# Performance work log

Measured on AMD Instinct MI355X. Metric: run time of the kernel, lower is better.

## Reference

```python
import jax, jax.numpy as jnp
import numpy as np

NUM_HEADS = 16
D_MODEL = 1024
HEAD_DIM = D_MODEL // NUM_HEADS
SCALE = float(np.sqrt(HEAD_DIM))  # NOTE: original multiplies q by sqrt(head_dim)
EPS = 1e-5


def layernorm(x, g, b):
    # LayerNorm over last dim (head_dim), learnable affine
    mu = jnp.mean(x, axis=-1, keepdims=True)
    var = jnp.mean(jnp.square(x - mu), axis=-1, keepdims=True)
    return (x - mu) * jax.lax.rsqrt(var + EPS) * g + b


def setup_inputs() -> dict:
    key = jax.random.key(0)
    ks = jax.random.split(key, 8)
    B, Nq, Nc = 2, 2048, 2048
    s = 0.02
    return {
        "x_query": jax.random.normal(ks[0], (B, Nq, D_MODEL), jnp.float32),
        "x_context": jax.random.normal(ks[1], (B, Nc, D_MODEL), jnp.float32),
        "Wq": jax.random.normal(ks[2], (D_MODEL, D_MODEL), jnp.float32) * s,
        "Wkv": jax.random.normal(ks[3], (D_MODEL, 2 * D_MODEL), jnp.float32) * s,
        "Wp": jax.random.normal(ks[4], (D_MODEL, D_MODEL), jnp.float32) * s,
        "bp": jnp.zeros((D_MODEL,), jnp.float32),
        "ln_g": jnp.ones((HEAD_DIM,), jnp.float32),
        "ln_b": jnp.zeros((HEAD_DIM,), jnp.float32),
    }


def reference(x_query, x_context, Wq, Wkv, Wp, bp, ln_g, ln_b):
    B, Nq, _ = x_query.shape
    Nc = x_context.shape[1]
    H, D = NUM_HEADS, HEAD_DIM
    # projections
    q = (x_query @ Wq).reshape(B, Nq, H, D).transpose(0, 2, 1, 3)  # b h n d
    kv = (x_context @ Wkv).reshape(B, Nc, 2, H, D)
    k = kv[:, :, 0].transpose(0, 2, 1, 3)  # b h n d
    v = kv[:, :, 1].transpose(0, 2, 1, 3)
    # QK-LayerNorm (shared params)
    q = layernorm(q, ln_g, ln_b)
    k = layernorm(k, ln_g, ln_b)
    # NOTE: faithful to source — q is MULTIPLIED by sqrt(head_dim)
    q = q * SCALE
    attn = jnp.einsum("bhqd,bhkd->bhqk", q, k)
    attn = jax.nn.softmax(attn, axis=-1)
    out = jnp.einsum("bhqk,bhkd->bhqd", attn, v)
    out = out.transpose(0, 2, 1, 3).reshape(B, Nq, H * D)
    return out @ Wp + bp
```

## Files before the change

### kernel.cpp

```cpp
#include <hip/hip_runtime.h>
#include <stdint.h>

#define NUM_HEADS 16
#define HEAD_DIM 64
#define D_MODEL 1024
#define SEQ 2048
#define BATCH 2

typedef unsigned short u16;
typedef _Float16 f16x8 __attribute__((ext_vector_type(8)));
typedef float f32x4 __attribute__((ext_vector_type(4)));

__device__ __forceinline__ u16 f2h(float f) {
    _Float16 h = (_Float16)f;
    return __builtin_bit_cast(u16, h);
}
__device__ __forceinline__ float h2f(u16 h) {
    return (float)__builtin_bit_cast(_Float16, h);
}
__device__ __forceinline__ uint32_t pkrtz(float a, float b) {
    return __builtin_bit_cast(uint32_t, __builtin_amdgcn_cvt_pkrtz(a, b));
}
__device__ __forceinline__ uint32_t pkrtn(float a, float b) {
    return (uint32_t)f2h(a) | ((uint32_t)f2h(b) << 16);
}

__device__ __forceinline__ float ex2(float x) {
#if __has_builtin(__builtin_amdgcn_exp2f)
    return __builtin_amdgcn_exp2f(x);
#else
    float r;
    asm("v_exp_f32 %0, %1" : "=v"(r) : "v"(x));
    return r;
#endif
}

__device__ __forceinline__ f16x8 ld8h(const u16* p) {
    return *reinterpret_cast<const f16x8*>(p);
}

__device__ __forceinline__ void gl_lds16(const void* g, void* l) {
    __builtin_amdgcn_global_load_lds(
        (const __attribute__((address_space(1))) void*)g,
        (__attribute__((address_space(3))) void*)l,
        16, 0, 0);
}

template <int CTRL>
__device__ __forceinline__ float dpp_mov(float x) {
    return __builtin_bit_cast(float,
        __builtin_amdgcn_update_dpp(0, __builtin_bit_cast(int, x), CTRL, 0xf, 0xf, true));
}
__device__ __forceinline__ float rowsum16(float x) {
    x += dpp_mov<0x121>(x);
    x += dpp_mov<0x122>(x);
    x += dpp_mov<0x124>(x);
    x += dpp_mov<0x128>(x);
    return x;
}

__global__ __launch_bounds__(256) void k_prep(const float* __restrict__ xq,
                                              const float* __restrict__ xc,
                                              const float* __restrict__ Wq,
                                              const float* __restrict__ Wkv,
                                              const float* __restrict__ Wp,
                                              u16* __restrict__ xq16,
                                              u16* __restrict__ xc16,
                                              u16* __restrict__ WqT16,
                                              u16* __restrict__ WkvT16,
                                              u16* __restrict__ WpT16) {
    __shared__ float tile[32][33];
    const int t = blockIdx.x;
    if (t < 8192) {
        int i = t * 256 + threadIdx.x;
        const float* src; u16* dst; int j;
        if (i < 1048576) { src = xq; dst = xq16; j = i; }
        else             { src = xc; dst = xc16; j = i - 1048576; }
        float4 v = reinterpret_cast<const float4*>(src)[j];
        ushort4 o;
        o.x = f2h(v.x); o.y = f2h(v.y); o.z = f2h(v.z); o.w = f2h(v.w);
        reinterpret_cast<ushort4*>(dst)[j] = o;
        return;
    }
    const float* W; u16* WT; int N, bi;
    if (t < 9216)       { W = Wq;  WT = WqT16;  N = 1024; bi = t - 8192; }
    else if (t < 11264) { W = Wkv; WT = WkvT16; N = 2048; bi = t - 9216; }
    else                { W = Wp;  WT = WpT16;  N = 1024; bi = t - 11264; }
    const int K = 1024;
    const int nb = N / 32;
    const int bn = (bi % nb) * 32, bk = (bi / nb) * 32;
    const int tx = threadIdx.x & 31;
    const int ty = threadIdx.x >> 5;
#pragma unroll
    for (int i = 0; i < 32; i += 8)
        tile[ty + i][tx] = W[(size_t)(bk + ty + i) * N + bn + tx];
    __syncthreads();
#pragma unroll
    for (int i = 0; i < 32; i += 8)
        WT[(size_t)(bn + ty + i) * K + bk + tx] = f2h(tile[tx][ty + i]);
}

__device__ __forceinline__ void gemm_mainloop_f16(const u16* __restrict__ A,
                                                  const u16* __restrict__ Bt,
                                                  u16* As, u16* Bs,
                                                  int tileM, int tileN, int K,
                                                  f32x4 acc[4][4]) {
    const int tid = threadIdx.x;
    const int lane = tid & 63;
    const int wv = tid >> 6;
    const int wm = wv >> 1, wn = wv & 1;
    const int quad = lane >> 4, l15 = lane & 15;

    const int c0 = tid, c1 = tid + 256;
    const u16* Ap0 = A + (size_t)(tileM + (c0 >> 2)) * K + (c0 & 3) * 8;
    const u16* Ap1 = A + (size_t)(tileM + (c1 >> 2)) * K + (c1 & 3) * 8;
    const u16* Bp0 = Bt + (size_t)(tileN + (c0 >> 2)) * K + (c0 & 3) * 8;
    const u16* Bp1 = Bt + (size_t)(tileN + (c1 >> 2)) * K + (c1 & 3) * 8;

    gl_lds16(Ap0, &As[c0 * 8]);
    gl_lds16(Ap1, &As[c1 * 8]);
    gl_lds16(Bp0, &Bs[c0 * 8]);
    gl_lds16(Bp1, &Bs[c1 * 8]);

    for (int k0 = 0; k0 < K; k0 += 32) {
        __syncthreads();
        const int cb = (k0 >> 5) & 1;
        if (k0 + 32 < K) {
            const int nbuf = cb ^ 1;
            gl_lds16(Ap0 + k0 + 32, &As[nbuf * 4096 + c0 * 8]);
            gl_lds16(Ap1 + k0 + 32, &As[nbuf * 4096 + c1 * 8]);
            gl_lds16(Bp0 + k0 + 32, &Bs[nbuf * 4096 + c0 * 8]);
            gl_lds16(Bp1 + k0 + 32, &Bs[nbuf * 4096 + c1 * 8]);
        }
        const int cbo = cb * 4096;
        f16x8 af[4], bfr[4];
#pragma unroll
        for (int mi = 0; mi < 4; ++mi)
            af[mi] = ld8h(&As[cbo + (wm * 64 + mi * 16 + l15) * 32 + quad * 8]);
#pragma unroll
        for (int ni = 0; ni < 4; ++ni)
            bfr[ni] = ld8h(&Bs[cbo + (wn * 64 + ni * 16 + l15) * 32 + quad * 8]);
#pragma unroll
        for (int mi = 0; mi < 4; ++mi)
#pragma unroll
            for (int ni = 0; ni < 4; ++ni)
                acc[mi][ni] = __builtin_amdgcn_mfma_f32_16x16x32_f16(
                    af[mi], bfr[ni], acc[mi][ni], 0, 0, 0);
    }
}

#define ACC_INIT()                                                   \
    f32x4 acc[4][4];                                                 \
    _Pragma("unroll") for (int i = 0; i < 4; ++i)                    \
        _Pragma("unroll") for (int j = 0; j < 4; ++j)                \
            acc[i][j] = (f32x4){0.f, 0.f, 0.f, 0.f};

__global__ __launch_bounds__(256, 2) void k_proj_f16(const u16* __restrict__ xq16,
                                                     const u16* __restrict__ xc16,
                                                     const u16* __restrict__ WqT16,
                                                     const u16* __restrict__ WkvT16,
                                                     const float* __restrict__ lng,
                                                     const float* __restrict__ lnb,
                                                     u16* __restrict__ Qh_h,
                                                     u16* __restrict__ Qh_l,
                                                     u16* __restrict__ Kh,
                                                     u16* __restrict__ VT) {
    __shared__ __align__(16) u16 As[2 * 128 * 32];
    __shared__ __align__(16) u16 Bs[2 * 128 * 32];
    const int bx = blockIdx.x;
    const int tileM = blockIdx.y * 128;
    const int tid = threadIdx.x;
    const int lane = tid & 63;
    const int wv = tid >> 6;
    const int wm = wv >> 1, wn = wv & 1;
    const int quad = lane >> 4, l15 = lane & 15;
    ACC_INIT();

    if (bx < 16) {
        const bool isQ = bx < 8;
        const int tileN = (bx & 7) * 128;
        const u16* Axx = isQ ? xq16 : xc16;
        const u16* Bt  = isQ ? WqT16 : WkvT16;
        const float scl = isQ ? 11.5415603294809528f : 1.0f;

        gemm_mainloop_f16(Axx, Bt, As, Bs, tileM, tileN, D_MODEL, acc);

        float gv[4], bv[4];
#pragma unroll
        for (int ni = 0; ni < 4; ++ni) { gv[ni] = lng[ni * 16 + l15]; bv[ni] = lnb[ni * 16 + l15]; }

        __syncthreads();
        u16* reg = (wv < 2 ? As : Bs) + (wv & 1) * 4096;
        const int h = (tileN + wn * 64) >> 6;
        const int mbase0 = tileM + wm * 64;
        const int bb = mbase0 >> 11;
        const size_t gb0 = (((size_t)bb * NUM_HEADS + h) * SEQ + (mbase0 & (SEQ - 1))) * HEAD_DIM;

#pragma unroll
        for (int mi = 0; mi < 4; ++mi) {
#pragma unroll
            for (int r = 0; r < 4; ++r) {
                float sum = 0.f, sq = 0.f;
#pragma unroll
                for (int ni = 0; ni < 4; ++ni) { float x = acc[mi][ni][r]; sum += x; sq += x * x; }
                sum = rowsum16(sum);
                sq  = rowsum16(sq);
                float mu = sum * (1.f / 64.f);
                float var = sq * (1.f / 64.f) - mu * mu;
                float rs = rsqrtf(var + 1e-5f);
                const int wrow = quad * 4 + r;
#pragma unroll
                for (int ni = 0; ni < 4; ++ni) {
                    float y = ((acc[mi][ni][r] - mu) * rs * gv[ni] + bv[ni]) * scl;
                    u16 yh = f2h(y);
                    reg[wrow * 64 + ni * 16 + l15] = yh;
                    if (isQ) reg[1024 + wrow * 64 + ni * 16 + l15] = f2h(y - h2f(yh));
                }
            }
            const size_t gmi = gb0 + (size_t)mi * 16 * 64;
#pragma unroll
            for (int p = 0; p < 2; ++p) {
                const int row = p * 8 + (lane >> 3);
                const int off = (lane & 7) * 8;
                uint4 vh = *reinterpret_cast<const uint4*>(&reg[row * 64 + off]);
                if (isQ) {
                    uint4 vl = *reinterpret_cast<const uint4*>(&reg[1024 + row * 64 + off]);
                    *reinterpret_cast<uint4*>(&Qh_h[gmi + row * 64 + off]) = vh;
                    *reinterpret_cast<uint4*>(&Qh_l[gmi + row * 64 + off]) = vl;
                } else {
                    *reinterpret_cast<uint4*>(&Kh[gmi + row * 64 + off]) = vh;
                }
            }
        }
    } else {
        const int tileN = D_MODEL + (bx - 16) * 128;
        gemm_mainloop_f16(xc16, WkvT16, As, Bs, tileM, tileN, D_MODEL, acc);

        __syncthreads();
        u16* reg = (wv < 2 ? As : Bs) + (wv & 1) * 4096;
#pragma unroll
        for (int mi = 0; mi < 4; ++mi) {
#pragma unroll
            for (int ni = 0; ni < 4; ++ni) {
                const int d = ni * 16 + l15;
                const int pc = (mi * 2 + (quad >> 1)) ^ (d & 7);
                ushort4 o;
                o.x = f2h(acc[mi][ni][0]);
                o.y = f2h(acc[mi][ni][1]);
                o.z = f2h(acc[mi][ni][2]);
                o.w = f2h(acc[mi][ni][3]);
                *reinterpret_cast<ushort4*>(&reg[d * 64 + pc * 8 + (quad & 1) * 4]) = o;
            }
        }
        const int h = (tileN + wn * 64 - D_MODEL) >> 6;
        const int m0 = tileM + wm * 64;
        const int bb = m0 >> 11, n0 = m0 & (SEQ - 1);
        const size_t vbase = (((size_t)bb * NUM_HEADS + h) * HEAD_DIM) * SEQ + n0;
#pragma unroll
        for (int p = 0; p < 8; ++p) {
            const int d = p * 8 + (lane >> 3);
            const int c = lane & 7;
            uint4 v = *reinterpret_cast<const uint4*>(&reg[d * 64 + ((c ^ (d & 7)) * 8)]);
            *reinterpret_cast<uint4*>(&VT[vbase + (size_t)d * SEQ + c * 8]) = v;
        }
    }
}

__global__ __launch_bounds__(256, 2) void k_gemm_out(const u16* __restrict__ A,
                                                     const u16* __restrict__ Bt,
                                                     const float* __restrict__ bp,
                                                     float* __restrict__ out) {
    __shared__ __align__(16) u16 As[2 * 128 * 32];
    __shared__ __align__(16) u16 Bs[2 * 128 * 32];
    const int tileM = blockIdx.y * 128, tileN = blockIdx.x * 128;
    const int tid = threadIdx.x;
    const int lane = tid & 63;
    const int wv = tid >> 6;
    const int wm = wv >> 1, wn = wv & 1;
    const int quad = lane >> 4, l15 = lane & 15;
    ACC_INIT();
    gemm_mainloop_f16(A, Bt, As, Bs, tileM, tileN, D_MODEL, acc);

    float bpv[4];
#pragma unroll
    for (int ni = 0; ni < 4; ++ni) bpv[ni] = bp[tileN + wn * 64 + ni * 16 + l15];
#pragma unroll
    for (int mi = 0; mi < 4; ++mi) {
#pragma unroll
        for (int r = 0; r < 4; ++r) {
            int m = tileM + wm * 64 + mi * 16 + quad * 4 + r;
#pragma unroll
            for (int ni = 0; ni < 4; ++ni) {
                int colg = tileN + wn * 64 + ni * 16 + l15;
                out[(size_t)m * D_MODEL + colg] = acc[mi][ni][r] + bpv[ni];
            }
        }
    }
}

__global__ __launch_bounds__(256) void k_attn(const u16* __restrict__ Qh_h,
                                              const u16* __restrict__ Qh_l,
                                              const u16* __restrict__ Kh,
                                              const u16* __restrict__ VT,
                                              u16* __restrict__ AO) {
    __shared__ __align__(16) u16 Ks[2 * 64 * 64];
    __shared__ __align__(16) u16 Vs[2 * 64 * 64];
    __shared__ __align__(16) u16 Ps[64 * 64];

    const int tid = threadIdx.x;
    const int lane = tid & 63;
    const int wv = tid >> 6;
    const int quad = lane >> 4, l15 = lane & 15;
    const int sw = l15 & 3;
    const int w1 = (l15 >> 2) & 1;
    const int id = blockIdx.x;
    const int bh = (id & 7) | (((id >> 7) & 3) << 3);
    const int qt = (id >> 3) & 15;

    const size_t bh_off = (size_t)bh * SEQ * HEAD_DIM;
    const u16* Vbh = VT + (size_t)bh * HEAD_DIM * SEQ;

    f16x8 qfh[2][2], qfl[2][2];
#pragma unroll
    for (int h = 0; h < 2; ++h)
#pragma unroll
        for (int kt = 0; kt < 2; ++kt) {
            size_t off = bh_off +
                (size_t)(qt * 128 + wv * 32 + h * 16 + l15) * HEAD_DIM + kt * 32 + quad * 8;
            qfh[h][kt] = ld8h(Qh_h + off);
            qfl[h][kt] = ld8h(Qh_l + off);
        }

    f16x8 ones;
#pragma unroll
    for (int i = 0; i < 8; ++i) ones[i] = (_Float16)1.0f;

    const int rr = lane >> 3;
    const int ss = lane & 7;
    const int cc = ss ^ rr;
    const int row0 = wv * 16 + rr;
    const u16* k0 = Kh + bh_off + (size_t)row0 * HEAD_DIM + cc * 8;
    const u16* v0 = Vbh + (size_t)row0 * SEQ + cc * 8;
    const int ldsW = (wv * 16) * 64;

    f32x4 acc_o[2][4];
    f32x4 acc_l0 = (f32x4){0.f, 0.f, 0.f, 0.f};
    f32x4 acc_l1 = (f32x4){0.f, 0.f, 0.f, 0.f};
    float m0 = -3.0e38f, m1 = -3.0e38f;
#pragma unroll
    for (int h = 0; h < 2; ++h)
#pragma unroll
        for (int ni = 0; ni < 4; ++ni) acc_o[h][ni] = (f32x4){0.f, 0.f, 0.f, 0.f};

    gl_lds16(k0,                &Ks[ldsW]);
    gl_lds16(k0 + 8 * HEAD_DIM, &Ks[ldsW + 8 * 64]);
    gl_lds16(v0,                &Vs[ldsW]);
    gl_lds16(v0 + 8 * SEQ,      &Vs[ldsW + 8 * 64]);

    const int psRow = (wv * 16 + l15) * 64;
    const int psX = (quad ^ (w1 << 1)) * 4;

    for (int j = 0; j < SEQ / 64; ++j) {
        __syncthreads();
        if (j + 1 < SEQ / 64) {
            const int nb = (j + 1) & 1;
            const size_t ko = (size_t)(j + 1) * 64 * HEAD_DIM;
            const int vo = (j + 1) * 64;
            gl_lds16(k0 + ko,                &Ks[nb * 4096 + ldsW]);
            gl_lds16(k0 + ko + 8 * HEAD_DIM, &Ks[nb * 4096 + ldsW + 8 * 64]);
            gl_lds16(v0 + vo,                &Vs[nb * 4096 + ldsW]);
            gl_lds16(v0 + vo + 8 * SEQ,      &Vs[nb * 4096 + ldsW + 8 * 64]);
        }
        const int bb = (j & 1) * 4096;

        f32x4 s0[4], s1[4];
#pragma unroll
        for (int ni = 0; ni < 4; ++ni) {
            s0[ni] = (f32x4){0.f, 0.f, 0.f, 0.f};
            s1[ni] = (f32x4){0.f, 0.f, 0.f, 0.f};
        }
#pragma unroll
        for (int kt = 0; kt < 2; ++kt) {
            f16x8 kf[4];
#pragma unroll
            for (int ni = 0; ni < 4; ++ni) {
                int slot = (kt * 4 + quad) ^ (l15 & 7);
                kf[ni] = ld8h(&Ks[bb + (ni * 16 + l15) * 64 + slot * 8]);
            }
#pragma unroll
            for (int ni = 0; ni < 4; ++ni) {
                s0[ni] = __builtin_amdgcn_mfma_f32_16x16x32_f16(
                    kf[ni], qfh[0][kt], s0[ni], 0, 0, 0);
                s0[ni] = __builtin_amdgcn_mfma_f32_16x16x32_f16(
                    kf[ni], qfl[0][kt], s0[ni], 0, 0, 0);
                s1[ni] = __builtin_amdgcn_mfma_f32_16x16x32_f16(
                    kf[ni], qfh[1][kt], s1[ni], 0, 0, 0);
                s1[ni] = __builtin_amdgcn_mfma_f32_16x16x32_f16(
                    kf[ni], qfl[1][kt], s1[ni], 0, 0, 0);
            }
        }

        float mxa[2];
#pragma unroll
        for (int h = 0; h < 2; ++h) {
            const f32x4* sh = h ? s1 : s0;
            float a = fmaxf(fmaxf(sh[0][0], sh[0][1]), fmaxf(sh[0][2], sh[0][3]));
            float b = fmaxf(fmaxf(sh[1][0], sh[1][1]), fmaxf(sh[1][2], sh[1][3]));
            float c = fmaxf(fmaxf(sh[2][0], sh[2][1]), fmaxf(sh[2][2], sh[2][3]));
            float d = fmaxf(fmaxf(sh[3][0], sh[3][1]), fmaxf(sh[3][2], sh[3][3]));
            float mx = fmaxf(fmaxf(a, b), fmaxf(c, d));
            mx = fmaxf(mx, __shfl_xor(mx, 16, 64));
            mx = fmaxf(mx, __shfl_xor(mx, 32, 64));
            mxa[h] = mx;
        }
        float mnew0 = fmaxf(m0, mxa[0]);
        float mnew1 = fmaxf(m1, mxa[1]);
        if (__any(fmaxf(mxa[0] - m0, mxa[1] - m1) > 0.f)) {
            float a0 = ex2(m0 - mnew0);
            float a1 = ex2(m1 - mnew1);
#pragma unroll
            for (int ni = 0; ni < 4; ++ni) { acc_o[0][ni] *= a0; acc_o[1][ni] *= a1; }
            acc_l0[0] *= a0;
            acc_l1[0] *= a1;
            m0 = mnew0;
            m1 = mnew1;
        }

#pragma unroll
        for (int ni = 0; ni < 4; ++ni) {
            uint2 u;
            u.x = pkrtz(ex2(s0[ni][0] - mnew0), ex2(s0[ni][1] - mnew0));
            u.y = pkrtz(ex2(s0[ni][2] - mnew0), ex2(s0[ni][3] - mnew0));
            *reinterpret_cast<uint2*>(&Ps[psRow + psX + ((ni ^ sw) * 16)]) = u;
        }
#pragma unroll
        for (int kt = 0; kt < 2; ++kt) {
            int pchunk = (kt * 2 + (quad >> 1)) ^ sw;
            int poff = pchunk * 16 + (((quad & 1) ^ w1) * 8);
            f16x8 pf = ld8h(&Ps[psRow + poff]);
            f16x8 vf[4];
#pragma unroll
            for (int ni = 0; ni < 4; ++ni) {
                int slot = (kt * 4 + quad) ^ (l15 & 7);
                vf[ni] = ld8h(&Vs[bb + (ni * 16 + l15) * 64 + slot * 8]);
            }
#pragma unroll
            for (int ni = 0; ni < 4; ++ni)
                acc_o[0][ni] = __builtin_amdgcn_mfma_f32_16x16x32_f16(
                    vf[ni], pf, acc_o[0][ni], 0, 0, 0);
            acc_l0 = __builtin_amdgcn_mfma_f32_16x16x32_f16(ones, pf, acc_l0, 0, 0, 0);
        }

#pragma unroll
        for (int ni = 0; ni < 4; ++ni) {
            uint2 u;
            u.x = pkrtz(ex2(s1[ni][0] - mnew1), ex2(s1[ni][1] - mnew1));
            u.y = pkrtz(ex2(s1[ni][2] - mnew1), ex2(s1[ni][3] - mnew1));
            *reinterpret_cast<uint2*>(&Ps[psRow + psX + ((ni ^ sw) * 16)]) = u;
        }
#pragma unroll
        for (int kt = 0; kt < 2; ++kt) {
            int pchunk = (kt * 2 + (quad >> 1)) ^ sw;
            int poff = pchunk * 16 + (((quad & 1) ^ w1) * 8);
            f16x8 pf = ld8h(&Ps[psRow + poff]);
            f16x8 vf[4];
#pragma unroll
            for (int ni = 0; ni < 4; ++ni) {
                int slot = (kt * 4 + quad) ^ (l15 & 7);
                vf[ni] = ld8h(&Vs[bb + (ni * 16 + l15) * 64 + slot * 8]);
            }
#pragma unroll
            for (int ni = 0; ni < 4; ++ni)
                acc_o[1][ni] = __builtin_amdgcn_mfma_f32_16x16x32_f16(
                    vf[ni], pf, acc_o[1][ni], 0, 0, 0);
            acc_l1 = __builtin_amdgcn_mfma_f32_16x16x32_f16(ones, pf, acc_l1, 0, 0, 0);
        }
    }

    const int b = bh >> 4, hh = bh & 15;
    const int echunk = quad ^ sw;
#pragma unroll
    for (int h = 0; h < 2; ++h) {
        const float inv = 1.0f / (h ? acc_l1[0] : acc_l0[0]);
        const f32x4* ao = acc_o[h];
#pragma unroll
        for (int ni = 0; ni < 4; ++ni) {
            uint2 u;
            u.x = pkrtn(ao[ni][0] * inv, ao[ni][1] * inv);
            u.y = pkrtn(ao[ni][2] * inv, ao[ni][3] * inv);
            *reinterpret_cast<uint2*>(&Ps[psRow + psX + ((ni ^ sw) * 16)]) = u;
        }
        const int qrow = qt * 128 + wv * 32 + h * 16 + l15;
        uint4 o0 = *reinterpret_cast<const uint4*>(&Ps[psRow + echunk * 16 + w1 * 8]);
        uint4 o1 = *reinterpret_cast<const uint4*>(&Ps[psRow + echunk * 16 + (1 - w1) * 8]);
        size_t outb = ((size_t)(b * SEQ + qrow)) * D_MODEL + hh * 64 + quad * 16;
        *reinterpret_cast<uint4*>(&AO[outb])     = o0;
        *reinterpret_cast<uint4*>(&AO[outb + 8]) = o1;
    }
}

extern "C" void kernel_launch(void* const* d_in, const int* in_sizes, int n_in,
                              void* d_out, int out_size, void* d_ws, size_t ws_size,
                              hipStream_t stream) {
    const float* xq  = (const float*)d_in[0];
    const float* xc  = (const float*)d_in[1];
    const float* Wq  = (const float*)d_in[2];
    const float* Wkv = (const float*)d_in[3];
    const float* Wp  = (const float*)d_in[4];
    const float* bp  = (const float*)d_in[5];
    const float* lng = (const float*)d_in[6];
    const float* lnb = (const float*)d_in[7];
    float* out = (float*)d_out;

    char* ws = (char*)d_ws;
    const size_t MB = 1 << 20;
    u16* xq16   = (u16*)(ws + 0 * MB);
    u16* xc16   = (u16*)(ws + 8 * MB);
    u16* WqT16  = (u16*)(ws + 16 * MB);
    u16* WkvT16 = (u16*)(ws + 18 * MB);
    u16* WpT16  = (u16*)(ws + 22 * MB);
    u16* Qh_h   = (u16*)(ws + 24 * MB);
    u16* Qh_l   = (u16*)(ws + 32 * MB);
    u16* Kh     = (u16*)(ws + 40 * MB);
    u16* VT     = (u16*)(ws + 48 * MB);
    u16* AO     = xq16;

    k_prep<<<12288, 256, 0, stream>>>(xq, xc, Wq, Wkv, Wp,
                                      xq16, xc16, WqT16, WkvT16, WpT16);
    k_proj_f16<<<dim3(24, 32), 256, 0, stream>>>(xq16, xc16, WqT16, WkvT16,
                                                 lng, lnb, Qh_h, Qh_l, Kh, VT);
    k_attn<<<512, 256, 0, stream>>>(Qh_h, Qh_l, Kh, VT, AO);
    k_gemm_out<<<dim3(8, 32), 256, 0, stream>>>(AO, WpT16, bp, out);
}
```

Before: 231.4 us.

## Split attention KV range in two and merge partials in a combine kernel

```diff
diff --git a/kernel.cpp b/kernel.cpp
--- a/kernel.cpp
+++ b/kernel.cpp
@@ -302,7 +302,9 @@
                                               const u16* __restrict__ Qh_l,
                                               const u16* __restrict__ Kh,
                                               const u16* __restrict__ VT,
-                                              u16* __restrict__ AO) {
+                                              u16* __restrict__ Op0,
+                                              u16* __restrict__ Op1,
+                                              float* __restrict__ ML) {
     __shared__ __align__(16) u16 Ks[2 * 64 * 64];
     __shared__ __align__(16) u16 Vs[2 * 64 * 64];
     __shared__ __align__(16) u16 Ps[64 * 64];
@@ -312,10 +314,12 @@
     const int wv = tid >> 6;
     const int quad = lane >> 4, l15 = lane & 15;
     const int sw = l15 & 3;
-    const int w1 = (l15 >> 2) & 1;
+    const int w1k = (l15 >> 2) & 1;
     const int id = blockIdx.x;
-    const int bh = (id & 7) | (((id >> 7) & 3) << 3);
-    const int qt = (id >> 3) & 15;
+    const int sp = id >> 9;
+    const int idr = id & 511;
+    const int bh = (idr & 7) | (((idr >> 7) & 3) << 3);
+    const int qt = (idr >> 3) & 15;
 
     const size_t bh_off = (size_t)bh * SEQ * HEAD_DIM;
     const u16* Vbh = VT + (size_t)bh * HEAD_DIM * SEQ;
@@ -339,8 +343,8 @@
     const int ss = lane & 7;
     const int cc = ss ^ rr;
     const int row0 = wv * 16 + rr;
-    const u16* k0 = Kh + bh_off + (size_t)row0 * HEAD_DIM + cc * 8;
-    const u16* v0 = Vbh + (size_t)row0 * SEQ + cc * 8;
+    const u16* k0 = Kh + bh_off + (size_t)(sp * 1024 + row0) * HEAD_DIM + cc * 8;
+    const u16* v0 = Vbh + (size_t)row0 * SEQ + sp * 1024 + cc * 8;
     const int ldsW = (wv * 16) * 64;
 
     f32x4 acc_o[2][4];
@@ -358,11 +362,12 @@
     gl_lds16(v0 + 8 * SEQ,      &Vs[ldsW + 8 * 64]);
 
     const int psRow = (wv * 16 + l15) * 64;
-    const int psX = (quad ^ (w1 << 1)) * 4;
-
-    for (int j = 0; j < SEQ / 64; ++j) {
+    const int psX = (quad ^ (w1k << 1)) * 4;
+
+    const int NT = 16;
+    for (int j = 0; j < NT; ++j) {
         __syncthreads();
-        if (j + 1 < SEQ / 64) {
+        if (j + 1 < NT) {
             const int nb = (j + 1) & 1;
             const size_t ko = (size_t)(j + 1) * 64 * HEAD_DIM;
             const int vo = (j + 1) * 64;
@@ -436,7 +441,7 @@
 #pragma unroll
         for (int kt = 0; kt < 2; ++kt) {
             int pchunk = (kt * 2 + (quad >> 1)) ^ sw;
-            int poff = pchunk * 16 + (((quad & 1) ^ w1) * 8);
+            int poff = pchunk * 16 + (((quad & 1) ^ w1k) * 8);
             f16x8 pf = ld8h(&Ps[psRow + poff]);
             f16x8 vf[4];
 #pragma unroll
@@ -461,7 +466,7 @@
 #pragma unroll
         for (int kt = 0; kt < 2; ++kt) {
             int pchunk = (kt * 2 + (quad >> 1)) ^ sw;
-            int poff = pchunk * 16 + (((quad & 1) ^ w1) * 8);
+            int poff = pchunk * 16 + (((quad & 1) ^ w1k) * 8);
             f16x8 pf = ld8h(&Ps[psRow + poff]);
             f16x8 vf[4];
 #pragma unroll
@@ -477,11 +482,13 @@
         }
     }
 
+    u16* Op = sp ? Op1 : Op0;
     const int b = bh >> 4, hh = bh & 15;
     const int echunk = quad ^ sw;
 #pragma unroll
     for (int h = 0; h < 2; ++h) {
-        const float inv = 1.0f / (h ? acc_l1[0] : acc_l0[0]);
+        const float lcur = h ? acc_l1[0] : acc_l0[0];
+        const float inv = 1.0f / lcur;
         const f32x4* ao = acc_o[h];
 #pragma unroll
         for (int ni = 0; ni < 4; ++ni) {
@@ -491,11 +498,51 @@
             *reinterpret_cast<uint2*>(&Ps[psRow + psX + ((ni ^ sw) * 16)]) = u;
         }
         const int qrow = qt * 128 + wv * 32 + h * 16 + l15;
-        uint4 o0 = *reinterpret_cast<const uint4*>(&Ps[psRow + echunk * 16 + w1 * 8]);
-        uint4 o1 = *reinterpret_cast<const uint4*>(&Ps[psRow + echunk * 16 + (1 - w1) * 8]);
+        if (quad == 0) {
+            const int midx = (sp * 32 + bh) * SEQ + qrow;
+            ML[midx] = h ? m1 : m0;
+            ML[131072 + midx] = lcur;
+        }
+        uint4 o0 = *reinterpret_cast<const uint4*>(&Ps[psRow + echunk * 16 + w1k * 8]);
+        uint4 o1 = *reinterpret_cast<const uint4*>(&Ps[psRow + echunk * 16 + (1 - w1k) * 8]);
         size_t outb = ((size_t)(b * SEQ + qrow)) * D_MODEL + hh * 64 + quad * 16;
-        *reinterpret_cast<uint4*>(&AO[outb])     = o0;
-        *reinterpret_cast<uint4*>(&AO[outb + 8]) = o1;
+        *reinterpret_cast<uint4*>(&Op[outb])     = o0;
+        *reinterpret_cast<uint4*>(&Op[outb + 8]) = o1;
+    }
+}
+
+__device__ __forceinline__ uint32_t comb2(uint32_t u1, uint32_t u2, float c1, float c2) {
+    float a0 = c1 * h2f((u16)(u1 & 0xffff)) + c2 * h2f((u16)(u2 & 0xffff));
+    float a1 = c1 * h2f((u16)(u1 >> 16)) + c2 * h2f((u16)(u2 >> 16));
+    return pkrtn(a0, a1);
+}
+__global__ __launch_bounds__(256) void k_comb(u16* __restrict__ O0,
+                                              const u16* __restrict__ O1,
+                                              const float* __restrict__ ML) {
+    const int bid = blockIdx.x;
+    const int bh = bid & 31, qc = bid >> 5;
+    const int b = bh >> 4, hh = bh & 15;
+    const int t = threadIdx.x;
+    const int q = qc * 128 + (t >> 1);
+    const int dp = (t & 1) * 32;
+    const int midx = bh * SEQ + q;
+    const float ma = ML[midx],          mb = ML[65536 + midx];
+    const float la = ML[131072 + midx], lb = ML[131072 + 65536 + midx];
+    const float M = fmaxf(ma, mb);
+    const float wa = ex2(ma - M) * la, wb = ex2(mb - M) * lb;
+    const float inv = 1.0f / (wa + wb);
+    const float c1 = wa * inv, c2 = wb * inv;
+    const size_t base = ((size_t)(b * SEQ + q)) * D_MODEL + hh * 64 + dp;
+#pragma unroll
+    for (int i = 0; i < 4; ++i) {
+        uint4 u1 = *reinterpret_cast<const uint4*>(&O0[base + i * 8]);
+        uint4 u2 = *reinterpret_cast<const uint4*>(&O1[base + i * 8]);
+        uint4 o;
+        o.x = comb2(u1.x, u2.x, c1, c2);
+        o.y = comb2(u1.y, u2.y, c1, c2);
+        o.z = comb2(u1.z, u2.z, c1, c2);
+        o.w = comb2(u1.w, u2.w, c1, c2);
+        *reinterpret_cast<uint4*>(&O0[base + i * 8]) = o;
     }
 }
 
@@ -523,12 +570,15 @@
     u16* Qh_l   = (u16*)(ws + 32 * MB);
     u16* Kh     = (u16*)(ws + 40 * MB);
     u16* VT     = (u16*)(ws + 48 * MB);
-    u16* AO     = xq16;
+    u16* Op0    = xq16;
+    u16* Op1    = xc16;
+    float* ML   = (float*)(ws + 16 * MB);
 
     k_prep<<<12288, 256, 0, stream>>>(xq, xc, Wq, Wkv, Wp,
                                       xq16, xc16, WqT16, WkvT16, WpT16);
     k_proj_f16<<<dim3(24, 32), 256, 0, stream>>>(xq16, xc16, WqT16, WkvT16,
                                                  lng, lnb, Qh_h, Qh_l, Kh, VT);
-    k_attn<<<512, 256, 0, stream>>>(Qh_h, Qh_l, Kh, VT, AO);
-    k_gemm_out<<<dim3(8, 32), 256, 0, stream>>>(AO, WpT16, bp, out);
-}
+    k_attn<<<1024, 256, 0, stream>>>(Qh_h, Qh_l, Kh, VT, Op0, Op1, ML);
+    k_comb<<<512, 256, 0, stream>>>(Op0, Op1, ML);
+    k_gemm_out<<<dim3(8, 32), 256, 0, stream>>>(Op0, WpT16, bp, out);
+}
```

Measured after the change: 240.7 us. 1.04x slower.
